# Optimization experiments

Hardware: AMD Instinct MI355X
Metric: run time of the kernel (lower is better)

The kernel has to match this reference:

```python
import jax, jax.numpy as jnp
import numpy as np

DECAY = 0.8      # cfg.ema_decay
EPS = 1e-5       # cfg.eps


def setup_inputs() -> dict:
    key = jax.random.key(0)
    k1, k2 = jax.random.split(key)
    H, B, N, D = 8, 8, 2048, 64   # num_codebooks, batch, seq, code_dim
    C = 1024                      # num_codes
    x = jax.random.normal(k1, (H, B, N, D), dtype=jnp.float32)
    embed = jax.random.normal(k2, (H, C, D), dtype=jnp.float32)
    embed_avg = embed.copy()
    cluster_size = jnp.ones((H, C), dtype=jnp.float32)
    return {"x": x, "embed": embed, "embed_avg": embed_avg, "cluster_size": cluster_size}


def reference(x, embed, embed_avg, cluster_size):
    # x: [h, b, n, d], embed: [h, c, d]
    h, b, n, d = x.shape
    c = embed.shape[1]
    flatten = x.reshape(h, b * n, d)  # pack 'h * d'

    # negative squared euclidean distance: -||f - e||^2
    f_sq = jnp.sum(flatten * flatten, axis=-1, keepdims=True)          # [h, N, 1]
    e_sq = jnp.sum(embed * embed, axis=-1)[:, None, :]                  # [h, 1, c]
    cross = jnp.einsum('hnd,hcd->hnc', flatten, embed)                  # [h, N, c]
    dist = -(f_sq - 2.0 * cross + e_sq)                                 # [h, N, c]

    # gumbel_sample with stochastic=False, straight_through=False -> argmax + one_hot
    embed_ind_flat = jnp.argmax(dist, axis=-1)                          # [h, N]
    embed_onehot = jax.nn.one_hot(embed_ind_flat, c, dtype=x.dtype)     # [h, N, c]

    # quantize (training path): onehot @ embed
    quantize = jnp.einsum('hnc,hcd->hnd', embed_onehot, embed).reshape(h, b, n, d)
    embed_ind = embed_ind_flat.reshape(h, b, n)

    # EMA codebook updates (ema_update=True, affine_params=False)
    cs_new = cluster_size * DECAY + embed_onehot.sum(axis=1) * (1.0 - DECAY)      # [h, c]
    embed_sum = jnp.einsum('hnd,hnc->hcd', flatten, embed_onehot)                  # [h, c, d]
    ea_new = embed_avg * DECAY + embed_sum * (1.0 - DECAY)                         # [h, c, d]

    ntot = jnp.sum(cs_new, axis=-1, keepdims=True)                                 # [h, 1]
    cs_smooth = (cs_new + EPS) / (ntot + c * EPS) * ntot                           # laplace smoothing * n
    embed_norm = ea_new / cs_smooth[..., None]                                     # new embed

    dist_out = dist.reshape(h, b, n, c)
    return quantize, embed_ind, embed_onehot, dist_out, embed_norm, ea_new, cs_new
```

## Files before the change

### kernel.cpp

```cpp
#include <hip/hip_runtime.h>

#define DECAY 0.8f
#define EPS   1e-5f
#define HN    8
#define BB    8
#define NSEQ  2048
#define DD    64
#define CC    1024
#define NROW  (BB*NSEQ)

#define XS(k,r) xs[(k)*128 + (r)]

typedef float vf4 __attribute__((ext_vector_type(4)));

__global__ void sumsq_kernel(const float* __restrict__ x, const float* __restrict__ embed,
                             float* __restrict__ fsq, float* __restrict__ esq) {
    int tid = blockIdx.x * blockDim.x + threadIdx.x;
    const int totalF = HN * NROW;
    const int totalE = HN * CC;
    if (tid < totalF) {
        const float4* src = (const float4*)(x + (size_t)tid * DD);
        float s = 0.f;
        #pragma unroll
        for (int i = 0; i < DD/4; ++i) {
            float4 v = src[i];
            s = fmaf(v.x, v.x, s); s = fmaf(v.y, v.y, s);
            s = fmaf(v.z, v.z, s); s = fmaf(v.w, v.w, s);
        }
        fsq[tid] = s;
    } else if (tid < totalF + totalE) {
        int t = tid - totalF;
        const float4* src = (const float4*)(embed + (size_t)t * DD);
        float s = 0.f;
        #pragma unroll
        for (int i = 0; i < DD/4; ++i) {
            float4 v = src[i];
            s = fmaf(v.x, v.x, s); s = fmaf(v.y, v.y, s);
            s = fmaf(v.z, v.z, s); s = fmaf(v.w, v.w, s);
        }
        esq[t] = s;
    }
}

__global__ __launch_bounds__(256)
void transpose_kernel(const float* __restrict__ e, float* __restrict__ eT) {
    __shared__ float t[64][68];
    const int h  = blockIdx.y;
    const int c0 = blockIdx.x * 64;
    const float* eh  = e  + (size_t)h * CC * DD;
    float*       eTh = eT + (size_t)h * DD * CC;
    const int r = threadIdx.x >> 4;
    const int q = threadIdx.x & 15;

    #pragma unroll
    for (int rr = 0; rr < 4; ++rr) {
        int cl = rr*16 + r;
        float4 v = *(const float4*)(eh + (size_t)(c0 + cl)*DD + q*4);
        t[q*4+0][cl] = v.x; t[q*4+1][cl] = v.y; t[q*4+2][cl] = v.z; t[q*4+3][cl] = v.w;
    }
    __syncthreads();
    #pragma unroll
    for (int rr = 0; rr < 4; ++rr) {
        int k = rr*16 + r;
        float4 w = *(const float4*)&t[k][q*4];
        *(float4*)(eTh + (size_t)k*CC + c0 + q*4) = w;
    }
}

__global__ __launch_bounds__(512, 4)
void dist_fp32_kernel(const float* __restrict__ x, const float* __restrict__ embed,
                      const float* __restrict__ eT,
                      const float* __restrict__ fsq, const float* __restrict__ esq,
                      float* __restrict__ out_q, float* __restrict__ out_i,
                      float* __restrict__ out_oh, float* __restrict__ out_d) {
    __shared__ float xs[64 * 128];

    const int h   = blockIdx.y;
    const int n0  = blockIdx.x * 128;
    const int tid = threadIdx.x;
    const int ty  = tid >> 4;
    const int tx  = tid & 15;

    const float* xh_   = x     + (size_t)h * NROW * DD;
    const float* eh_   = embed + (size_t)h * CC   * DD;
    const float* eT_h  = eT    + (size_t)h * DD   * CC;
    const float* esq_h = esq   + h * CC;

    {
        const int g4 = (tid & 31) * 4;
        const int k0 = (tid >> 5) * 4;
        float4 v[4];
        #pragma unroll
        for (int i = 0; i < 4; ++i)
            v[i] = *(const float4*)(xh_ + (size_t)(n0 + g4 + i) * DD + k0);
        *(float4*)&XS(k0+0, g4) = make_float4(v[0].x, v[1].x, v[2].x, v[3].x);
        *(float4*)&XS(k0+1, g4) = make_float4(v[0].y, v[1].y, v[2].y, v[3].y);
        *(float4*)&XS(k0+2, g4) = make_float4(v[0].z, v[1].z, v[2].z, v[3].z);
        *(float4*)&XS(k0+3, g4) = make_float4(v[0].w, v[1].w, v[2].w, v[3].w);
    }
    asm volatile("s_waitcnt lgkmcnt(0)" ::: "memory");
    __builtin_amdgcn_s_barrier();

    float fs[4];
    #pragma unroll
    for (int i = 0; i < 4; ++i) fs[i] = fsq[h*NROW + n0 + ty*4 + i];

    float bestv[4];
    int   besti[4];
    #pragma unroll
    for (int i = 0; i < 4; ++i) { bestv[i] = -3.4e38f; besti[i] = 0; }

    #pragma unroll 1
    for (int ci = 0; ci < 8; ++ci) {
        const int c0 = ci * 128;
        const float* bbase = eT_h + c0 + tx*8;

        float acc[4][8];
        #pragma unroll
        for (int i = 0; i < 4; ++i)
            #pragma unroll
            for (int j = 0; j < 8; ++j) acc[i][j] = 0.f;

        #pragma unroll 4
        for (int k = 0; k < 64; ++k) {
            float a[4], b[8];
            *(float4*)&a[0] = *(const float4*)&XS(k, ty*4);
            *(float4*)&b[0] = *(const float4*)(bbase + (size_t)k*CC);
            *(float4*)&b[4] = *(const float4*)(bbase + (size_t)k*CC + 4);
            #pragma unroll
            for (int i = 0; i < 4; ++i)
                #pragma unroll
                for (int j = 0; j < 8; ++j)
                    acc[i][j] = fmaf(a[i], b[j], acc[i][j]);
        }

        float eq[8];
        *(float4*)&eq[0] = *(const float4*)(esq_h + c0 + tx*8);
        *(float4*)&eq[4] = *(const float4*)(esq_h + c0 + tx*8 + 4);

        const vf4 z = {0.f, 0.f, 0.f, 0.f};
        #pragma unroll
        for (int i = 0; i < 4; ++i) {
            int row = n0 + ty*4 + i;
            float dv[8];
            #pragma unroll
            for (int j = 0; j < 8; ++j)
                dv[j] = fmaf(2.f, acc[i][j], -(fs[i] + eq[j]));

            size_t rb = ((size_t)h*NROW + row)*CC + c0 + tx*8;
            vf4 d0 = {dv[0], dv[1], dv[2], dv[3]};
            vf4 d1 = {dv[4], dv[5], dv[6], dv[7]};
            __builtin_nontemporal_store(d0, (vf4*)(out_d + rb));
            __builtin_nontemporal_store(d1, (vf4*)(out_d + rb + 4));
            __builtin_nontemporal_store(z,  (vf4*)(out_oh + rb));
            __builtin_nontemporal_store(z,  (vf4*)(out_oh + rb + 4));

            #pragma unroll
            for (int j = 0; j < 8; ++j) {
                if (dv[j] > bestv[i]) { bestv[i] = dv[j]; besti[i] = c0 + tx*8 + j; }
            }
        }
    }

    asm volatile("s_waitcnt vmcnt(0)" ::: "memory");

    #pragma unroll
    for (int i = 0; i < 4; ++i) {
        float v  = bestv[i];
        int   id = besti[i];
        #pragma unroll
        for (int off = 8; off >= 1; off >>= 1) {
            float ov = __shfl_xor(v, off, 64);
            int   oi = __shfl_xor(id, off, 64);
            if (ov > v || (ov == v && oi < id)) { v = ov; id = oi; }
        }
        int row = n0 + ty*4 + i;
        float4 qv = *(const float4*)(eh_ + (size_t)id*DD + tx*4);
        *(float4*)(out_q + ((size_t)h*NROW + row)*DD + tx*4) = qv;
        if (tx == 0) {
            out_i[(size_t)h*NROW + row] = (float)id;
            out_oh[((size_t)h*NROW + row)*CC + id] = 1.0f;
        }
    }
}

__global__ __launch_bounds__(64)
void ema_kernel(const float* __restrict__ x, const float* __restrict__ embed_avg,
                const float* __restrict__ cluster_size, const float* __restrict__ ind_f,
                float* __restrict__ out_cs, float* __restrict__ out_ea,
                float* __restrict__ out_norm) {
    const int h    = blockIdx.y;
    const int c    = blockIdx.x;
    const int lane = threadIdx.x;

    const float* cs_h = cluster_size + h*CC;
    float s = 0.f;
    #pragma unroll
    for (int i = 0; i < CC/64; ++i) s += cs_h[lane + i*64];
    #pragma unroll
    for (int off = 32; off >= 1; off >>= 1) s += __shfl_xor(s, off, 64);

    const float* xh   = x     + (size_t)h * NROW * DD;
    const float* indh = ind_f + (size_t)h * NROW;

    float sum_d = 0.f;
    int   cnt   = 0;
    for (int chunk = 0; chunk < NROW/64; ++chunk) {
        int myidx = (int)indh[chunk*64 + lane];
        unsigned long long m = __ballot(myidx == c);
        while (m) {
            int t = __ffsll(m) - 1;
            m &= m - 1;
            int n = chunk*64 + t;
            sum_d += xh[(size_t)n*DD + lane];
            cnt++;
        }
    }

    float csn  = cs_h[c]*DECAY + (float)cnt*(1.f - DECAY);
    float ea   = embed_avg[((size_t)h*CC + c)*DD + lane]*DECAY + sum_d*(1.f - DECAY);
    float ntot = s*DECAY + (1.f - DECAY)*(float)NROW;
    float css  = (csn + EPS) / (ntot + (float)CC*EPS) * ntot;

    out_ea  [((size_t)h*CC + c)*DD + lane] = ea;
    out_norm[((size_t)h*CC + c)*DD + lane] = ea / css;
    if (lane == 0) out_cs[h*CC + c] = csn;
}

extern "C" void kernel_launch(void* const* d_in, const int* in_sizes, int n_in,
                              void* d_out, int out_size, void* d_ws, size_t ws_size,
                              hipStream_t stream) {
    const float* x            = (const float*)d_in[0];
    const float* embed        = (const float*)d_in[1];
    const float* embed_avg    = (const float*)d_in[2];
    const float* cluster_size = (const float*)d_in[3];

    float* out = (float*)d_out;
    float* fsq = (float*)d_ws;
    float* esq = fsq + (size_t)HN * NROW;
    float* eT  = esq + (size_t)HN * CC;

    float* out_q    = out;
    float* out_i    = out_q    + (size_t)HN * NROW * DD;
    float* out_oh   = out_i    + (size_t)HN * NROW;
    float* out_d    = out_oh   + (size_t)HN * NROW * CC;
    float* out_norm = out_d    + (size_t)HN * NROW * CC;
    float* out_ea   = out_norm + (size_t)HN * CC * DD;
    float* out_cs   = out_ea   + (size_t)HN * CC * DD;

    {
        int total = HN*NROW + HN*CC;
        sumsq_kernel<<<(total + 255)/256, 256, 0, stream>>>(x, embed, fsq, esq);
    }
    {
        dim3 g(CC/64, HN);
        transpose_kernel<<<g, 256, 0, stream>>>(embed, eT);
    }
    {
        dim3 g(NROW/128, HN);
        dist_fp32_kernel<<<g, 512, 0, stream>>>(x, embed, eT, fsq, esq,
                                                out_q, out_i, out_oh, out_d);
    }
    {
        dim3 g(CC, HN);
        ema_kernel<<<g, 64, 0, stream>>>(x, embed_avg, cluster_size, out_i,
                                         out_cs, out_ea, out_norm);
    }
}
```

Baseline: 633.3 us.

## Stage codebook tiles in LDS with register prefetch; memset one-hot buffer separately

Removes the separate transpose kernel and instead loads each 128-code embed tile into shared memory, transposed in registers, prefetching the next tile during the current tile's FMA loop. The zeroing of the one-hot output moves out of the distance kernel into a hipMemsetAsync, and the distance stores become plain stores in a split column layout (tx*4 and 64+tx*4) so LDS reads avoid bank conflicts. This trades global/L2 reads of eT for LDS traffic plus two barriers per tile. It also adds a separate full pass to zero the 64 MB one-hot buffer, which may cost more than the in-kernel zero stores it replaces.

```diff
diff --git a/kernel.cpp b/kernel.cpp
--- a/kernel.cpp
+++ b/kernel.cpp
@@ -9,7 +9,9 @@
 #define CC    1024
 #define NROW  (BB*NSEQ)
 
-#define XS(k,r) xs[(k)*128 + (r)]
+#define LS 128
+#define XS(k,r) xs[(k)*LS + (r)]
+#define ES(k,c) es[(k)*LS + (c)]
 
 typedef float vf4 __attribute__((ext_vector_type(4)));
 
@@ -42,38 +44,13 @@
     }
 }
 
-__global__ __launch_bounds__(256)
-void transpose_kernel(const float* __restrict__ e, float* __restrict__ eT) {
-    __shared__ float t[64][68];
-    const int h  = blockIdx.y;
-    const int c0 = blockIdx.x * 64;
-    const float* eh  = e  + (size_t)h * CC * DD;
-    float*       eTh = eT + (size_t)h * DD * CC;
-    const int r = threadIdx.x >> 4;
-    const int q = threadIdx.x & 15;
-
-    #pragma unroll
-    for (int rr = 0; rr < 4; ++rr) {
-        int cl = rr*16 + r;
-        float4 v = *(const float4*)(eh + (size_t)(c0 + cl)*DD + q*4);
-        t[q*4+0][cl] = v.x; t[q*4+1][cl] = v.y; t[q*4+2][cl] = v.z; t[q*4+3][cl] = v.w;
-    }
-    __syncthreads();
-    #pragma unroll
-    for (int rr = 0; rr < 4; ++rr) {
-        int k = rr*16 + r;
-        float4 w = *(const float4*)&t[k][q*4];
-        *(float4*)(eTh + (size_t)k*CC + c0 + q*4) = w;
-    }
-}
-
 __global__ __launch_bounds__(512, 4)
 void dist_fp32_kernel(const float* __restrict__ x, const float* __restrict__ embed,
-                      const float* __restrict__ eT,
                       const float* __restrict__ fsq, const float* __restrict__ esq,
                       float* __restrict__ out_q, float* __restrict__ out_i,
                       float* __restrict__ out_oh, float* __restrict__ out_d) {
-    __shared__ float xs[64 * 128];
+    __shared__ float xs[64 * LS];
+    __shared__ float es[64 * LS];
 
     const int h   = blockIdx.y;
     const int n0  = blockIdx.x * 128;
@@ -83,12 +60,12 @@
 
     const float* xh_   = x     + (size_t)h * NROW * DD;
     const float* eh_   = embed + (size_t)h * CC   * DD;
-    const float* eT_h  = eT    + (size_t)h * DD   * CC;
     const float* esq_h = esq   + h * CC;
 
-    {
-        const int g4 = (tid & 31) * 4;
-        const int k0 = (tid >> 5) * 4;
+    const int g4 = (tid & 31) * 4;
+    const int k0 = (tid >> 5) * 4;
+
+    {
         float4 v[4];
         #pragma unroll
         for (int i = 0; i < 4; ++i)
@@ -98,6 +75,16 @@
         *(float4*)&XS(k0+2, g4) = make_float4(v[0].z, v[1].z, v[2].z, v[3].z);
         *(float4*)&XS(k0+3, g4) = make_float4(v[0].w, v[1].w, v[2].w, v[3].w);
     }
+    {
+        float4 v[4];
+        #pragma unroll
+        for (int i = 0; i < 4; ++i)
+            v[i] = *(const float4*)(eh_ + (size_t)(g4 + i) * DD + k0);
+        *(float4*)&ES(k0+0, g4) = make_float4(v[0].x, v[1].x, v[2].x, v[3].x);
+        *(float4*)&ES(k0+1, g4) = make_float4(v[0].y, v[1].y, v[2].y, v[3].y);
+        *(float4*)&ES(k0+2, g4) = make_float4(v[0].z, v[1].z, v[2].z, v[3].z);
+        *(float4*)&ES(k0+3, g4) = make_float4(v[0].w, v[1].w, v[2].w, v[3].w);
+    }
     asm volatile("s_waitcnt lgkmcnt(0)" ::: "memory");
     __builtin_amdgcn_s_barrier();
 
@@ -113,7 +100,13 @@
     #pragma unroll 1
     for (int ci = 0; ci < 8; ++ci) {
         const int c0 = ci * 128;
-        const float* bbase = eT_h + c0 + tx*8;
+
+        float4 ev[4];
+        if (ci < 7) {
+            #pragma unroll
+            for (int i = 0; i < 4; ++i)
+                ev[i] = *(const float4*)(eh_ + (size_t)(c0 + 128 + g4 + i) * DD + k0);
+        }
 
         float acc[4][8];
         #pragma unroll
@@ -125,8 +118,8 @@
         for (int k = 0; k < 64; ++k) {
             float a[4], b[8];
             *(float4*)&a[0] = *(const float4*)&XS(k, ty*4);
-            *(float4*)&b[0] = *(const float4*)(bbase + (size_t)k*CC);
-            *(float4*)&b[4] = *(const float4*)(bbase + (size_t)k*CC + 4);
+            *(float4*)&b[0] = *(const float4*)&ES(k, tx*4);
+            *(float4*)&b[4] = *(const float4*)&ES(k, 64 + tx*4);
             #pragma unroll
             for (int i = 0; i < 4; ++i)
                 #pragma unroll
@@ -135,10 +128,9 @@
         }
 
         float eq[8];
-        *(float4*)&eq[0] = *(const float4*)(esq_h + c0 + tx*8);
-        *(float4*)&eq[4] = *(const float4*)(esq_h + c0 + tx*8 + 4);
-
-        const vf4 z = {0.f, 0.f, 0.f, 0.f};
+        *(float4*)&eq[0] = *(const float4*)(esq_h + c0 + tx*4);
+        *(float4*)&eq[4] = *(const float4*)(esq_h + c0 + 64 + tx*4);
+
         #pragma unroll
         for (int i = 0; i < 4; ++i) {
             int row = n0 + ty*4 + i;
@@ -147,22 +139,34 @@
             for (int j = 0; j < 8; ++j)
                 dv[j] = fmaf(2.f, acc[i][j], -(fs[i] + eq[j]));
 
-            size_t rb = ((size_t)h*NROW + row)*CC + c0 + tx*8;
+            size_t rb = ((size_t)h*NROW + row)*CC + c0;
             vf4 d0 = {dv[0], dv[1], dv[2], dv[3]};
             vf4 d1 = {dv[4], dv[5], dv[6], dv[7]};
-            __builtin_nontemporal_store(d0, (vf4*)(out_d + rb));
-            __builtin_nontemporal_store(d1, (vf4*)(out_d + rb + 4));
-            __builtin_nontemporal_store(z,  (vf4*)(out_oh + rb));
-            __builtin_nontemporal_store(z,  (vf4*)(out_oh + rb + 4));
-
-            #pragma unroll
-            for (int j = 0; j < 8; ++j) {
-                if (dv[j] > bestv[i]) { bestv[i] = dv[j]; besti[i] = c0 + tx*8 + j; }
+            *(vf4*)(out_d + rb + tx*4)      = d0;
+            *(vf4*)(out_d + rb + 64 + tx*4) = d1;
+
+            #pragma unroll
+            for (int j = 0; j < 4; ++j) {
+                if (dv[j] > bestv[i]) { bestv[i] = dv[j]; besti[i] = c0 + tx*4 + j; }
             }
-        }
-    }
-
-    asm volatile("s_waitcnt vmcnt(0)" ::: "memory");
+            #pragma unroll
+            for (int j = 4; j < 8; ++j) {
+                if (dv[j] > bestv[i]) { bestv[i] = dv[j]; besti[i] = c0 + 64 + tx*4 + (j-4); }
+            }
+        }
+
+        if (ci < 7) {
+            asm volatile("s_waitcnt lgkmcnt(0)" ::: "memory");
+            __builtin_amdgcn_s_barrier();
+            *(float4*)&ES(k0+0, g4) = make_float4(ev[0].x, ev[1].x, ev[2].x, ev[3].x);
+            *(float4*)&ES(k0+1, g4) = make_float4(ev[0].y, ev[1].y, ev[2].y, ev[3].y);
+            *(float4*)&ES(k0+2, g4) = make_float4(ev[0].z, ev[1].z, ev[2].z, ev[3].z);
+            *(float4*)&ES(k0+3, g4) = make_float4(ev[0].w, ev[1].w, ev[2].w, ev[3].w);
+            asm volatile("s_waitcnt lgkmcnt(0)" ::: "memory");
+            __builtin_amdgcn_s_barrier();
+        }
+    }
+
 
     #pragma unroll
     for (int i = 0; i < 4; ++i) {
@@ -238,7 +242,6 @@
     float* out = (float*)d_out;
     float* fsq = (float*)d_ws;
     float* esq = fsq + (size_t)HN * NROW;
-    float* eT  = esq + (size_t)HN * CC;
 
     float* out_q    = out;
     float* out_i    = out_q    + (size_t)HN * NROW * DD;
@@ -248,17 +251,15 @@
     float* out_ea   = out_norm + (size_t)HN * CC * DD;
     float* out_cs   = out_ea   + (size_t)HN * CC * DD;
 
+    hipMemsetAsync(out_oh, 0, (size_t)HN * NROW * CC * sizeof(float), stream);
+
     {
         int total = HN*NROW + HN*CC;
         sumsq_kernel<<<(total + 255)/256, 256, 0, stream>>>(x, embed, fsq, esq);
     }
     {
-        dim3 g(CC/64, HN);
-        transpose_kernel<<<g, 256, 0, stream>>>(embed, eT);
-    }
-    {
         dim3 g(NROW/128, HN);
-        dist_fp32_kernel<<<g, 512, 0, stream>>>(x, embed, eT, fsq, esq,
+        dist_fp32_kernel<<<g, 512, 0, stream>>>(x, embed, fsq, esq,
                                                 out_q, out_i, out_oh, out_d);
     }
     {
```

New measurement: 643.8 us. About the same (+1.7%).
